# Optimization experiments

Measured on AMD Instinct MI355X. Metric: run time of the kernel, lower is better.

The kernel has to match this reference:

```python
import jax, jax.numpy as jnp
import numpy as np

N = 50000      # nodes
E = 400000     # edges (before self-loops)
D_IN = 128     # input node features
H1, C1 = 8, 64   # layer-1 heads / per-head channels (concat -> 512)
H2, C2 = 1, 16   # layer-2 heads / per-head channels (mean -> 16)
NEG_SLOPE = 0.2  # PyG GATConv default leaky-relu slope


def setup_inputs() -> dict:
    key = jax.random.key(0)
    ks = jax.random.split(key, 10)
    x = jax.random.normal(ks[0], (N, D_IN), jnp.float32)
    edge_index = jax.random.randint(ks[1], (2, E), 0, N, dtype=jnp.int32)
    s1 = D_IN ** -0.5
    s2 = (H1 * C1) ** -0.5
    return {
        "x": x,
        "edge_index": edge_index,
        "W1": jax.random.normal(ks[2], (D_IN, H1 * C1), jnp.float32) * s1,
        "a1_src": jax.random.normal(ks[3], (H1, C1), jnp.float32) * (C1 ** -0.5),
        "a1_dst": jax.random.normal(ks[4], (H1, C1), jnp.float32) * (C1 ** -0.5),
        "b1": jnp.zeros((H1 * C1,), jnp.float32),
        "W2": jax.random.normal(ks[5], (H1 * C1, H2 * C2), jnp.float32) * s2,
        "a2_src": jax.random.normal(ks[6], (H2, C2), jnp.float32) * (C2 ** -0.5),
        "a2_dst": jax.random.normal(ks[7], (H2, C2), jnp.float32) * (C2 ** -0.5),
        "b2": jnp.zeros((C2,), jnp.float32),
    }


def gat_layer(x, W, a_src, a_dst, bias, src, dst, H, C, concat):
    n = x.shape[0]
    h = (x @ W).reshape(n, H, C)                       # [N,H,C]
    # per-node attention halves (PyG: alpha = a_src . h_src + a_dst . h_dst)
    al_src = jnp.einsum('nhc,hc->nh', h, a_src)        # [N,H]
    al_dst = jnp.einsum('nhc,hc->nh', h, a_dst)
    logits = jax.nn.leaky_relu(al_src[src] + al_dst[dst], NEG_SLOPE)  # [E,H]
    # segment softmax over incoming edges of each destination node
    m = jax.ops.segment_max(logits, dst, num_segments=n)
    e = jnp.exp(logits - m[dst])
    denom = jax.ops.segment_sum(e, dst, num_segments=n)
    alpha = e / denom[dst]                             # [E,H]
    out = jax.ops.segment_sum(alpha[:, :, None] * h[src], dst, num_segments=n)  # [N,H,C]
    out = out.reshape(n, H * C) if concat else out.mean(axis=1)
    return out + bias


def reference(x, edge_index, W1, a1_src, a1_dst, b1, W2, a2_src, a2_dst, b2):
    n = x.shape[0]
    # PyG GATConv adds self-loops by default (applied in each layer)
    loops = jnp.arange(n, dtype=edge_index.dtype)
    src = jnp.concatenate([edge_index[0], loops])
    dst = jnp.concatenate([edge_index[1], loops])
    h1 = gat_layer(x, W1, a1_src, a1_dst, b1, src, dst, H1, C1, True)   # [N,512]
    h1 = jax.nn.elu(h1)
    return gat_layer(h1, W2, a2_src, a2_dst, b2, src, dst, H2, C2, False)  # [N,16]
```

## Files before the change

kernel.cpp:

```cpp
#include <hip/hip_runtime.h>
#include <math.h>

#define N_NODES 50000
#define N_EDGES 400000
#define N_TOT   450000
#define NEG 0.2f
#define CAP 64

typedef __attribute__((ext_vector_type(8))) short bf16x8;
typedef __attribute__((ext_vector_type(8))) unsigned short u16x8;
typedef __attribute__((ext_vector_type(4))) float f32x4;

__device__ __forceinline__ float lrelu(float x) { return x > 0.f ? x : NEG * x; }

__device__ __forceinline__ unsigned short f2bf(float f) {
    unsigned u = __float_as_uint(f);
    unsigned r = u + 0x7FFFu + ((u >> 16) & 1u);
    return (unsigned short)(r >> 16);
}
__device__ __forceinline__ float bf2f(unsigned short h) {
    return __uint_as_float(((unsigned)h) << 16);
}

__global__ void k_init(const float* __restrict__ W1, unsigned short* W1hiT,
                       const float* __restrict__ W2, unsigned short* W2hiT,
                       const float* __restrict__ a1s, const float* __restrict__ a1d,
                       unsigned short* W1aThi, unsigned short* W1aTlo,
                       int* cursor) {
    int i = blockIdx.x * 256 + threadIdx.x;
    if (i < 128 * 512) {
        int col = i & 511, k = i >> 9;
        W1hiT[col * 128 + k] = f2bf(W1[k * 512 + col]);
    } else if (i < 128 * 512 + 512 * 16) {
        int j = i - 128 * 512;
        int col = j & 15, k = j >> 4;
        W2hiT[col * 512 + k] = f2bf(W2[k * 16 + col]);
    } else if (i < 128 * 512 + 512 * 16 + 128 * 16) {
        int j = i - (128 * 512 + 512 * 16);
        int c16 = j & 15, k = j >> 4;
        int hd = c16 & 7;
        const float* av = (c16 < 8) ? a1s : a1d;
        float acc = 0.f;
#pragma unroll 8
        for (int c = 0; c < 64; c++)
            acc = fmaf(W1[k * 512 + hd * 64 + c], av[hd * 64 + c], acc);
        unsigned short h = f2bf(acc);
        W1aThi[c16 * 128 + k] = h;
        W1aTlo[c16 * 128 + k] = f2bf(acc - bf2f(h));
    } else {
        int j = i - (128 * 512 + 512 * 16 + 128 * 16);
        if (j < N_NODES) cursor[j] = 0;
    }
}

#define SCAT 256
__global__ __launch_bounds__(256) void k_sg1(const int* __restrict__ ei,
                                             int* __restrict__ cursor,
                                             int* __restrict__ colsrc,
                                             const float* __restrict__ x,
                                             const unsigned short* __restrict__ W1hiT,
                                             const unsigned short* __restrict__ W1aThi,
                                             const unsigned short* __restrict__ W1aTlo,
                                             unsigned short* __restrict__ h1b,
                                             float* __restrict__ al1s,
                                             float* __restrict__ al1d) {
    __shared__ unsigned short xs_hi[64 * 136];
    if (blockIdx.x < SCAT) {
        int gtid = blockIdx.x * 256 + threadIdx.x;
        for (int i = gtid; i < N_TOT; i += SCAT * 256) {
            int src, dst;
            if (i < N_EDGES) { src = ei[i]; dst = ei[N_EDGES + i]; }
            else             { src = dst = i - N_EDGES; }
            int pos = atomicAdd(&cursor[dst], 1);
            if (pos < CAP) colsrc[dst * CAP + pos] = src;
        }
        return;
    }
    const int t = threadIdx.x;
    const int rb = (blockIdx.x - SCAT) * 64;

#pragma unroll
    for (int i = 0; i < 8; i++) {
        int idx = t + 256 * i;
        int r = idx >> 5;
        int k = (idx & 31) * 4;
        int gr = rb + r;
        float4 v = make_float4(0.f, 0.f, 0.f, 0.f);
        if (gr < N_NODES) v = *reinterpret_cast<const float4*>(&x[gr * 128 + k]);
        ushort4 hi;
        hi.x = f2bf(v.x); hi.y = f2bf(v.y); hi.z = f2bf(v.z); hi.w = f2bf(v.w);
        *reinterpret_cast<ushort4*>(&xs_hi[r * 136 + k]) = hi;
    }
    __syncthreads();

    const int lane = t & 63;
    const int w = t >> 6;
    const int kbase = (lane >> 4) * 8;
    const int colloc = (w << 4) + (lane & 15);

#pragma unroll
    for (int pr = 0; pr < 4; pr++) {
        bf16x8 bhi[2][4];
#pragma unroll
        for (int si = 0; si < 2; si++) {
            int col = (pr * 2 + si) * 64 + colloc;
#pragma unroll
            for (int kc = 0; kc < 4; kc++)
                bhi[si][kc] = *reinterpret_cast<const bf16x8*>(&W1hiT[col * 128 + kc * 32 + kbase]);
        }
#pragma unroll
        for (int mt = 0; mt < 4; mt++) {
            const int arow = mt * 16 + (lane & 15);
            bf16x8 ah[4];
#pragma unroll
            for (int kc = 0; kc < 4; kc++)
                ah[kc] = *reinterpret_cast<const bf16x8*>(&xs_hi[arow * 136 + kc * 32 + kbase]);
#pragma unroll
            for (int si = 0; si < 2; si++) {
                f32x4 acc = {0.f, 0.f, 0.f, 0.f};
#pragma unroll
                for (int kc = 0; kc < 4; kc++)
                    acc = __builtin_amdgcn_mfma_f32_16x16x32_bf16(ah[kc], bhi[si][kc], acc, 0, 0, 0);
                const int col = (pr * 2 + si) * 64 + colloc;
                const int r0 = rb + mt * 16 + (lane >> 4) * 4;
#pragma unroll
                for (int r = 0; r < 4; r++) {
                    int row = r0 + r;
                    if (row < N_NODES) h1b[row * 512 + col] = f2bf(acc[r]);
                }
            }
        }
    }

    {
        const int c16 = lane & 15;
        bf16x8 bh[4], bl[4];
#pragma unroll
        for (int kc = 0; kc < 4; kc++) {
            bh[kc] = *reinterpret_cast<const bf16x8*>(&W1aThi[c16 * 128 + kc * 32 + kbase]);
            bl[kc] = *reinterpret_cast<const bf16x8*>(&W1aTlo[c16 * 128 + kc * 32 + kbase]);
        }
        const int arow = (w << 4) + (lane & 15);
        f32x4 acc = {0.f, 0.f, 0.f, 0.f};
#pragma unroll
        for (int kc = 0; kc < 4; kc++) {
            bf16x8 ah = *reinterpret_cast<const bf16x8*>(&xs_hi[arow * 136 + kc * 32 + kbase]);
            acc = __builtin_amdgcn_mfma_f32_16x16x32_bf16(ah, bh[kc], acc, 0, 0, 0);
            acc = __builtin_amdgcn_mfma_f32_16x16x32_bf16(ah, bl[kc], acc, 0, 0, 0);
        }
        const int r0 = rb + (w << 4) + (lane >> 4) * 4;
#pragma unroll
        for (int r = 0; r < 4; r++) {
            int row = r0 + r;
            if (row < N_NODES) {
                if (c16 < 8) al1s[row * 8 + c16] = acc[r];
                else         al1d[row * 8 + (c16 - 8)] = acc[r];
            }
        }
    }
}

__global__ __launch_bounds__(256) void k_agg1(const int* __restrict__ cursor,
                                              const int* __restrict__ colsrc,
                                              const float* __restrict__ al1s,
                                              const float* __restrict__ al1d,
                                              const unsigned short* __restrict__ h1b,
                                              const float* __restrict__ b1,
                                              const unsigned short* __restrict__ W2hiT,
                                              const float* __restrict__ a2s,
                                              const float* __restrict__ a2d,
                                              unsigned short* __restrict__ h2b,
                                              float* __restrict__ al2s,
                                              float* __restrict__ al2d) {
    __shared__ float pw[4][8 * 66];
    __shared__ __align__(16) unsigned short vs[4 * 520];
    const int wid  = threadIdx.x >> 6;
    const int lane = threadIdx.x & 63;
    const int n0 = blockIdx.x * 4;
    const int n  = n0 + wid;
    const int cnt = min(cursor[n], CAP);
    const int eb = n * CAP;
    const int h  = lane >> 3;
    const int c8 = lane << 3;
    float* mypw = pw[wid];

    const float4 d0 = *reinterpret_cast<const float4*>(&al1d[n * 8]);
    const float4 d1 = *reinterpret_cast<const float4*>(&al1d[n * 8 + 4]);

    int s0 = 0;
    float p[8];
    if (lane < cnt) {
        s0 = colsrc[eb + lane];
        const float4 u0 = *reinterpret_cast<const float4*>(&al1s[s0 * 8]);
        const float4 u1 = *reinterpret_cast<const float4*>(&al1s[s0 * 8 + 4]);
        p[0] = __expf(fminf(lrelu(u0.x + d0.x), 60.f));
        p[1] = __expf(fminf(lrelu(u0.y + d0.y), 60.f));
        p[2] = __expf(fminf(lrelu(u0.z + d0.z), 60.f));
        p[3] = __expf(fminf(lrelu(u0.w + d0.w), 60.f));
        p[4] = __expf(fminf(lrelu(u1.x + d1.x), 60.f));
        p[5] = __expf(fminf(lrelu(u1.y + d1.y), 60.f));
        p[6] = __expf(fminf(lrelu(u1.z + d1.z), 60.f));
        p[7] = __expf(fminf(lrelu(u1.w + d1.w), 60.f));
    } else {
#pragma unroll
        for (int hh = 0; hh < 8; hh++) p[hh] = 0.f;
    }
#pragma unroll
    for (int hh = 0; hh < 8; hh++) mypw[hh * 66 + lane] = p[hh];

    float acc[8] = {0.f, 0.f, 0.f, 0.f, 0.f, 0.f, 0.f, 0.f};
    float sm = 0.f;
    const int pwh = h * 66;

    int j = 0;
    for (; j + 3 < cnt; j += 4) {
        int sa = __shfl(s0, j,     64);
        int sb = __shfl(s0, j + 1, 64);
        int sc = __shfl(s0, j + 2, 64);
        int sd = __shfl(s0, j + 3, 64);
        u16x8 va = *reinterpret_cast<const u16x8*>(&h1b[sa * 512 + c8]);
        u16x8 vb = *reinterpret_cast<const u16x8*>(&h1b[sb * 512 + c8]);
        u16x8 vc = *reinterpret_cast<const u16x8*>(&h1b[sc * 512 + c8]);
        u16x8 vd = *reinterpret_cast<const u16x8*>(&h1b[sd * 512 + c8]);
        float wa = mypw[pwh + j];
        float wb = mypw[pwh + j + 1];
        float wc = mypw[pwh + j + 2];
        float wd = mypw[pwh + j + 3];
        sm += (wa + wb) + (wc + wd);
#pragma unroll
        for (int k = 0; k < 8; k++) {
            float t0 = fmaf(wa, bf2f(va[k]), acc[k]);
            t0 = fmaf(wb, bf2f(vb[k]), t0);
            t0 = fmaf(wc, bf2f(vc[k]), t0);
            acc[k] = fmaf(wd, bf2f(vd[k]), t0);
        }
    }
    for (; j < cnt; ++j) {
        int s = __shfl(s0, j, 64);
        u16x8 v = *reinterpret_cast<const u16x8*>(&h1b[s * 512 + c8]);
        float w = mypw[pwh + j];
        sm += w;
#pragma unroll
        for (int k = 0; k < 8; k++) acc[k] = fmaf(w, bf2f(v[k]), acc[k]);
    }

    const float inv = 1.f / sm;
    const float4 ba = *reinterpret_cast<const float4*>(&b1[c8]);
    const float4 bb = *reinterpret_cast<const float4*>(&b1[c8 + 4]);
    float v[8];
    v[0] = acc[0] * inv + ba.x; v[1] = acc[1] * inv + ba.y;
    v[2] = acc[2] * inv + ba.z; v[3] = acc[3] * inv + ba.w;
    v[4] = acc[4] * inv + bb.x; v[5] = acc[5] * inv + bb.y;
    v[6] = acc[6] * inv + bb.z; v[7] = acc[7] * inv + bb.w;
#pragma unroll
    for (int k = 0; k < 8; k++)
        v[k] = v[k] > 0.f ? v[k] : __expf(v[k]) - 1.f;
    u16x8 o;
#pragma unroll
    for (int k = 0; k < 8; k++) o[k] = f2bf(v[k]);
    *reinterpret_cast<u16x8*>(&vs[wid * 520 + c8]) = o;

    __syncthreads();

    if (wid == 0) {
        const int col   = lane & 15;
        const int kbase = (lane >> 4) << 3;
        const int rowm  = lane & 3;
        f32x4 a2 = {0.f, 0.f, 0.f, 0.f};
#pragma unroll 4
        for (int kc = 0; kc < 16; kc++) {
            bf16x8 bh = *reinterpret_cast<const bf16x8*>(&W2hiT[col * 512 + kc * 32 + kbase]);
            bf16x8 ah = *reinterpret_cast<const bf16x8*>(&vs[rowm * 520 + kc * 32 + kbase]);
            a2 = __builtin_amdgcn_mfma_f32_16x16x32_bf16(ah, bh, a2, 0, 0, 0);
        }
        if (lane < 16) {
            const float as_c = a2s[col];
            const float ad_c = a2d[col];
#pragma unroll
            for (int r = 0; r < 4; r++) {
                float ps = a2[r] * as_c;
                float pd = a2[r] * ad_c;
                ps += __shfl_xor(ps, 1, 64); pd += __shfl_xor(pd, 1, 64);
                ps += __shfl_xor(ps, 2, 64); pd += __shfl_xor(pd, 2, 64);
                ps += __shfl_xor(ps, 4, 64); pd += __shfl_xor(pd, 4, 64);
                ps += __shfl_xor(ps, 8, 64); pd += __shfl_xor(pd, 8, 64);
                h2b[(n0 + r) * 16 + col] = f2bf(a2[r]);
                if (lane == 0) { al2s[n0 + r] = ps; al2d[n0 + r] = pd; }
            }
        }
    }
}

__global__ __launch_bounds__(256) void k_agg2(const int* __restrict__ cursor,
                                              const int* __restrict__ colsrc,
                                              const float* __restrict__ al2s,
                                              const float* __restrict__ al2d,
                                              const unsigned short* __restrict__ h2b,
                                              const float* __restrict__ b2,
                                              float* __restrict__ out) {
    int wv = threadIdx.x >> 6, lane = threadIdx.x & 63;
    int n = blockIdx.x * 4 + wv;
    if (n >= N_NODES) return;
    int cnt = min(cursor[n], CAP);
    const int eb = n * CAP;
    float ald = al2d[n];
    int c = lane & 15, q = lane >> 4;
    float acc = 0.f, smL = 0.f;
    int e = q;
    for (; e + 4 < cnt; e += 8) {
        int s0 = colsrc[eb + e];
        int s1 = colsrc[eb + e + 4];
        float w0 = __expf(fminf(lrelu(al2s[s0] + ald), 60.f));
        float w1 = __expf(fminf(lrelu(al2s[s1] + ald), 60.f));
        unsigned short v0 = h2b[s0 * 16 + c];
        unsigned short v1 = h2b[s1 * 16 + c];
        smL += w0 + w1;
        acc = fmaf(w0, bf2f(v0), acc);
        acc = fmaf(w1, bf2f(v1), acc);
    }
    for (; e < cnt; e += 4) {
        int s = colsrc[eb + e];
        float w = __expf(fminf(lrelu(al2s[s] + ald), 60.f));
        smL += w;
        acc = fmaf(w, bf2f(h2b[s * 16 + c]), acc);
    }
    acc += __shfl_xor(acc, 16, 64); smL += __shfl_xor(smL, 16, 64);
    acc += __shfl_xor(acc, 32, 64); smL += __shfl_xor(smL, 32, 64);
    if (q == 0) out[n * 16 + c] = acc / smL + b2[c];
}

extern "C" void kernel_launch(void* const* d_in, const int* in_sizes, int n_in,
                              void* d_out, int out_size, void* d_ws, size_t ws_size,
                              hipStream_t stream) {
    const float* x   = (const float*)d_in[0];
    const int*   ei  = (const int*)d_in[1];
    const float* W1  = (const float*)d_in[2];
    const float* a1s = (const float*)d_in[3];
    const float* a1d = (const float*)d_in[4];
    const float* b1  = (const float*)d_in[5];
    const float* W2  = (const float*)d_in[6];
    const float* a2s = (const float*)d_in[7];
    const float* a2d = (const float*)d_in[8];
    const float* b2  = (const float*)d_in[9];
    float* out = (float*)d_out;

    char* ws = (char*)d_ws;
    unsigned short* h1b = (unsigned short*)(ws + 0);
    unsigned short* h2b = (unsigned short*)(ws + 102400000);
    float* al1s = (float*)(ws + 105600000);
    float* al1d = (float*)(ws + 107200000);
    float* al2s = (float*)(ws + 108800000);
    float* al2d = (float*)(ws + 109000000);
    int* cursor = (int*)(ws + 109200000);
    int* colsrc = (int*)(ws + 109400000);
    unsigned short* W1hiT  = (unsigned short*)(ws + 122200000);
    unsigned short* W2hiT  = (unsigned short*)(ws + 122336000);
    unsigned short* W1aThi = (unsigned short*)(ws + 122352384);
    unsigned short* W1aTlo = (unsigned short*)(ws + 122356480);

    k_init<<<492, 256, 0, stream>>>(W1, W1hiT, W2, W2hiT, a1s, a1d, W1aThi, W1aTlo, cursor);

    k_sg1<<<SCAT + (N_NODES + 63) / 64, 256, 0, stream>>>(ei, cursor, colsrc, x,
                                                          W1hiT, W1aThi, W1aTlo,
                                                          h1b, al1s, al1d);

    k_agg1<<<(N_NODES + 3) / 4, 256, 0, stream>>>(cursor, colsrc, al1s, al1d, h1b, b1,
                                                  W2hiT, a2s, a2d, h2b, al2s, al2d);

    k_agg2<<<(N_NODES + 3) / 4, 256, 0, stream>>>(cursor, colsrc, al2s, al2d, h2b, b2, out);
}
```

Measured before the change: 218.8 us.

## Split layer-1 aggregation across two waves per node and widen layer-2 edge parallelism

k_agg1 now uses 512-thread blocks with two waves per destination node. Each wave handles four heads (256 channels) with 4-wide bf16 loads. The edge loop is padded to multiples of 8 with zero weights so eight gathers are in flight at once. k_agg2 now processes eight edges per iteration across lane groups, with each lane reading two channels as one 32-bit load. The aim is more memory-level parallelism and occupancy for the gather-bound aggregation, at the cost of duplicated index and weight work and some wasted padded loads.

```diff
diff --git a/kernel.cpp b/kernel.cpp
--- a/kernel.cpp
+++ b/kernel.cpp
@@ -160,7 +160,7 @@
     }
 }
 
-__global__ __launch_bounds__(256) void k_agg1(const int* __restrict__ cursor,
+__global__ __launch_bounds__(512) void k_agg1(const int* __restrict__ cursor,
                                               const int* __restrict__ colsrc,
                                               const float* __restrict__ al1s,
                                               const float* __restrict__ al1d,
@@ -174,95 +174,76 @@
                                               float* __restrict__ al2d) {
     __shared__ float pw[4][8 * 66];
     __shared__ __align__(16) unsigned short vs[4 * 520];
-    const int wid  = threadIdx.x >> 6;
+    const int wv   = threadIdx.x >> 6;
     const int lane = threadIdx.x & 63;
+    const int nd   = wv >> 1;
+    const int half = wv & 1;
     const int n0 = blockIdx.x * 4;
-    const int n  = n0 + wid;
+    const int n  = n0 + nd;
     const int cnt = min(cursor[n], CAP);
     const int eb = n * CAP;
-    const int h  = lane >> 3;
-    const int c8 = lane << 3;
-    float* mypw = pw[wid];
-
-    const float4 d0 = *reinterpret_cast<const float4*>(&al1d[n * 8]);
-    const float4 d1 = *reinterpret_cast<const float4*>(&al1d[n * 8 + 4]);
+    const int h  = half * 4 + (lane >> 4);
+    const int c4 = half * 256 + lane * 4;
+    float* mypw = pw[nd];
+
+    const float4 dh = *reinterpret_cast<const float4*>(&al1d[n * 8 + half * 4]);
 
     int s0 = 0;
-    float p[8];
+    float p0 = 0.f, p1 = 0.f, p2 = 0.f, p3 = 0.f;
     if (lane < cnt) {
         s0 = colsrc[eb + lane];
-        const float4 u0 = *reinterpret_cast<const float4*>(&al1s[s0 * 8]);
-        const float4 u1 = *reinterpret_cast<const float4*>(&al1s[s0 * 8 + 4]);
-        p[0] = __expf(fminf(lrelu(u0.x + d0.x), 60.f));
-        p[1] = __expf(fminf(lrelu(u0.y + d0.y), 60.f));
-        p[2] = __expf(fminf(lrelu(u0.z + d0.z), 60.f));
-        p[3] = __expf(fminf(lrelu(u0.w + d0.w), 60.f));
-        p[4] = __expf(fminf(lrelu(u1.x + d1.x), 60.f));
-        p[5] = __expf(fminf(lrelu(u1.y + d1.y), 60.f));
-        p[6] = __expf(fminf(lrelu(u1.z + d1.z), 60.f));
-        p[7] = __expf(fminf(lrelu(u1.w + d1.w), 60.f));
-    } else {
-#pragma unroll
-        for (int hh = 0; hh < 8; hh++) p[hh] = 0.f;
-    }
-#pragma unroll
-    for (int hh = 0; hh < 8; hh++) mypw[hh * 66 + lane] = p[hh];
-
-    float acc[8] = {0.f, 0.f, 0.f, 0.f, 0.f, 0.f, 0.f, 0.f};
-    float sm = 0.f;
+        const float4 u = *reinterpret_cast<const float4*>(&al1s[s0 * 8 + half * 4]);
+        p0 = __expf(fminf(lrelu(u.x + dh.x), 60.f));
+        p1 = __expf(fminf(lrelu(u.y + dh.y), 60.f));
+        p2 = __expf(fminf(lrelu(u.z + dh.z), 60.f));
+        p3 = __expf(fminf(lrelu(u.w + dh.w), 60.f));
+    }
+    mypw[(half * 4 + 0) * 66 + lane] = p0;
+    mypw[(half * 4 + 1) * 66 + lane] = p1;
+    mypw[(half * 4 + 2) * 66 + lane] = p2;
+    mypw[(half * 4 + 3) * 66 + lane] = p3;
+
+    float acc0 = 0.f, acc1 = 0.f, acc2 = 0.f, acc3 = 0.f, sm = 0.f;
     const int pwh = h * 66;
-
-    int j = 0;
-    for (; j + 3 < cnt; j += 4) {
-        int sa = __shfl(s0, j,     64);
-        int sb = __shfl(s0, j + 1, 64);
-        int sc = __shfl(s0, j + 2, 64);
-        int sd = __shfl(s0, j + 3, 64);
-        u16x8 va = *reinterpret_cast<const u16x8*>(&h1b[sa * 512 + c8]);
-        u16x8 vb = *reinterpret_cast<const u16x8*>(&h1b[sb * 512 + c8]);
-        u16x8 vc = *reinterpret_cast<const u16x8*>(&h1b[sc * 512 + c8]);
-        u16x8 vd = *reinterpret_cast<const u16x8*>(&h1b[sd * 512 + c8]);
-        float wa = mypw[pwh + j];
-        float wb = mypw[pwh + j + 1];
-        float wc = mypw[pwh + j + 2];
-        float wd = mypw[pwh + j + 3];
-        sm += (wa + wb) + (wc + wd);
+    const int cnt8 = (cnt + 7) & ~7;
+
+    for (int j = 0; j < cnt8; j += 8) {
+        int s[8]; float w[8]; ushort4 vv[8];
 #pragma unroll
         for (int k = 0; k < 8; k++) {
-            float t0 = fmaf(wa, bf2f(va[k]), acc[k]);
-            t0 = fmaf(wb, bf2f(vb[k]), t0);
-            t0 = fmaf(wc, bf2f(vc[k]), t0);
-            acc[k] = fmaf(wd, bf2f(vd[k]), t0);
-        }
-    }
-    for (; j < cnt; ++j) {
-        int s = __shfl(s0, j, 64);
-        u16x8 v = *reinterpret_cast<const u16x8*>(&h1b[s * 512 + c8]);
-        float w = mypw[pwh + j];
-        sm += w;
-#pragma unroll
-        for (int k = 0; k < 8; k++) acc[k] = fmaf(w, bf2f(v[k]), acc[k]);
+            s[k] = __shfl(s0, j + k, 64);
+            w[k] = mypw[pwh + j + k];
+        }
+#pragma unroll
+        for (int k = 0; k < 8; k++)
+            vv[k] = *reinterpret_cast<const ushort4*>(&h1b[s[k] * 512 + c4]);
+#pragma unroll
+        for (int k = 0; k < 8; k++) {
+            sm += w[k];
+            acc0 = fmaf(w[k], bf2f(vv[k].x), acc0);
+            acc1 = fmaf(w[k], bf2f(vv[k].y), acc1);
+            acc2 = fmaf(w[k], bf2f(vv[k].z), acc2);
+            acc3 = fmaf(w[k], bf2f(vv[k].w), acc3);
+        }
     }
 
     const float inv = 1.f / sm;
-    const float4 ba = *reinterpret_cast<const float4*>(&b1[c8]);
-    const float4 bb = *reinterpret_cast<const float4*>(&b1[c8 + 4]);
-    float v[8];
-    v[0] = acc[0] * inv + ba.x; v[1] = acc[1] * inv + ba.y;
-    v[2] = acc[2] * inv + ba.z; v[3] = acc[3] * inv + ba.w;
-    v[4] = acc[4] * inv + bb.x; v[5] = acc[5] * inv + bb.y;
-    v[6] = acc[6] * inv + bb.z; v[7] = acc[7] * inv + bb.w;
-#pragma unroll
-    for (int k = 0; k < 8; k++)
-        v[k] = v[k] > 0.f ? v[k] : __expf(v[k]) - 1.f;
-    u16x8 o;
-#pragma unroll
-    for (int k = 0; k < 8; k++) o[k] = f2bf(v[k]);
-    *reinterpret_cast<u16x8*>(&vs[wid * 520 + c8]) = o;
+    const float4 bb = *reinterpret_cast<const float4*>(&b1[c4]);
+    float v0 = acc0 * inv + bb.x;
+    float v1 = acc1 * inv + bb.y;
+    float v2 = acc2 * inv + bb.z;
+    float v3 = acc3 * inv + bb.w;
+    v0 = v0 > 0.f ? v0 : __expf(v0) - 1.f;
+    v1 = v1 > 0.f ? v1 : __expf(v1) - 1.f;
+    v2 = v2 > 0.f ? v2 : __expf(v2) - 1.f;
+    v3 = v3 > 0.f ? v3 : __expf(v3) - 1.f;
+    ushort4 o;
+    o.x = f2bf(v0); o.y = f2bf(v1); o.z = f2bf(v2); o.w = f2bf(v3);
+    *reinterpret_cast<ushort4*>(&vs[nd * 520 + c4]) = o;
 
     __syncthreads();
 
-    if (wid == 0) {
+    if (wv == 0) {
         const int col   = lane & 15;
         const int kbase = (lane >> 4) << 3;
         const int rowm  = lane & 3;
@@ -304,29 +285,27 @@
     int cnt = min(cursor[n], CAP);
     const int eb = n * CAP;
     float ald = al2d[n];
-    int c = lane & 15, q = lane >> 4;
-    float acc = 0.f, smL = 0.f;
-    int e = q;
-    for (; e + 4 < cnt; e += 8) {
-        int s0 = colsrc[eb + e];
-        int s1 = colsrc[eb + e + 4];
-        float w0 = __expf(fminf(lrelu(al2s[s0] + ald), 60.f));
-        float w1 = __expf(fminf(lrelu(al2s[s1] + ald), 60.f));
-        unsigned short v0 = h2b[s0 * 16 + c];
-        unsigned short v1 = h2b[s1 * 16 + c];
-        smL += w0 + w1;
-        acc = fmaf(w0, bf2f(v0), acc);
-        acc = fmaf(w1, bf2f(v1), acc);
-    }
-    for (; e < cnt; e += 4) {
+    int q = lane >> 3;
+    int c2 = (lane & 7) << 1;
+    float acc0 = 0.f, acc1 = 0.f, smL = 0.f;
+    for (int e = q; e < cnt; e += 8) {
         int s = colsrc[eb + e];
         float w = __expf(fminf(lrelu(al2s[s] + ald), 60.f));
+        unsigned v = *reinterpret_cast<const unsigned*>(&h2b[s * 16 + c2]);
         smL += w;
-        acc = fmaf(w, bf2f(h2b[s * 16 + c]), acc);
-    }
-    acc += __shfl_xor(acc, 16, 64); smL += __shfl_xor(smL, 16, 64);
-    acc += __shfl_xor(acc, 32, 64); smL += __shfl_xor(smL, 32, 64);
-    if (q == 0) out[n * 16 + c] = acc / smL + b2[c];
+        acc0 = fmaf(w, bf2f((unsigned short)(v & 0xFFFFu)), acc0);
+        acc1 = fmaf(w, __uint_as_float(v & 0xFFFF0000u), acc1);
+    }
+    acc0 += __shfl_xor(acc0, 8, 64);  acc1 += __shfl_xor(acc1, 8, 64);  smL += __shfl_xor(smL, 8, 64);
+    acc0 += __shfl_xor(acc0, 16, 64); acc1 += __shfl_xor(acc1, 16, 64); smL += __shfl_xor(smL, 16, 64);
+    acc0 += __shfl_xor(acc0, 32, 64); acc1 += __shfl_xor(acc1, 32, 64); smL += __shfl_xor(smL, 32, 64);
+    if (q == 0) {
+        float inv = 1.f / smL;
+        float2 r;
+        r.x = acc0 * inv + b2[c2];
+        r.y = acc1 * inv + b2[c2 + 1];
+        *reinterpret_cast<float2*>(&out[n * 16 + c2]) = r;
+    }
 }
 
 extern "C" void kernel_launch(void* const* d_in, const int* in_sizes, int n_in,
@@ -364,7 +343,7 @@
                                                           W1hiT, W1aThi, W1aTlo,
                                                           h1b, al1s, al1d);
 
-    k_agg1<<<(N_NODES + 3) / 4, 256, 0, stream>>>(cursor, colsrc, al1s, al1d, h1b, b1,
+    k_agg1<<<(N_NODES + 3) / 4, 512, 0, stream>>>(cursor, colsrc, al1s, al1d, h1b, b1,
                                                   W2hiT, a2s, a2d, h2b, al2s, al2d);
 
     k_agg2<<<(N_NODES + 3) / 4, 256, 0, stream>>>(cursor, colsrc, al2s, al2d, h2b, b2, out);
```

After: 230.5 us. 1.05x slower.
